# Kernel tuning notes

Hardware: AMD Instinct MI355X
Metric: run time of the kernel (lower is better)

Reference implementation:

```python
import jax, jax.numpy as jnp
import numpy as np
from jax import lax

# Production-scale RPN detection-head config
B, FH, FW, NA = 8, 200, 200, 9      # batch, fmap h, fmap w, anchors/cell
H, W = 800, 800                      # image dims
N = FH * FW * NA                     # 360k anchors per image
NMS_THR = 0.7
MIN_SIZE = 1e-3


def _make_anchors():
    scales = np.array([32.0, 64.0, 128.0])
    ratios = np.array([0.5, 1.0, 2.0])
    ws = (scales[:, None] * np.sqrt(1.0 / ratios)[None, :]).reshape(-1)  # [NA]
    hs = (scales[:, None] * np.sqrt(ratios)[None, :]).reshape(-1)
    sy, sx = H / FH, W / FW
    cx = (np.arange(FW) + 0.5) * sx
    cy = (np.arange(FH) + 0.5) * sy
    cxg, cyg = np.meshgrid(cx, cy)                     # [FH,FW]
    cxg = cxg[..., None]; cyg = cyg[..., None]         # [FH,FW,1]
    a = np.stack([cxg - ws / 2, cyg - hs / 2, cxg + ws / 2, cyg + hs / 2], axis=-1)
    return jnp.asarray(a.reshape(-1, 4), jnp.float32)  # [N,4] xyxy


def setup_inputs() -> dict:
    key = jax.random.key(0)
    k1, k2 = jax.random.split(key)
    cls_logits = jax.random.normal(k1, (B, N, 1), jnp.float32)
    reg_deltas = jax.random.normal(k2, (B, N, 4), jnp.float32) * 0.1  # sane exp(dw)
    anchors = jnp.broadcast_to(_make_anchors()[None], (B, N, 4))
    return {
        "cls_logits": cls_logits,
        "reg_deltas": reg_deltas,
        "anchors": anchors,
        "keep_pre_nms": 1000,
        "keep_post_nms": 300,
    }


def _offsets2boxes(deltas, anchors):
    aw = anchors[:, 2] - anchors[:, 0]
    ah = anchors[:, 3] - anchors[:, 1]
    acx = anchors[:, 0] + 0.5 * aw
    acy = anchors[:, 1] + 0.5 * ah
    cx = deltas[:, 0] * aw + acx
    cy = deltas[:, 1] * ah + acy
    w = jnp.exp(deltas[:, 2]) * aw
    h = jnp.exp(deltas[:, 3]) * ah
    return jnp.stack([cx - 0.5 * w, cy - 0.5 * h, cx + 0.5 * w, cy + 0.5 * h], axis=-1)


def _iou_matrix(b):
    area = (b[:, 2] - b[:, 0]) * (b[:, 3] - b[:, 1])
    lt = jnp.maximum(b[:, None, :2], b[None, :, :2])
    rb = jnp.minimum(b[:, None, 2:], b[None, :, 2:])
    wh = jnp.clip(rb - lt, 0.0)
    inter = wh[..., 0] * wh[..., 1]
    return inter / (area[:, None] + area[None, :] - inter + 1e-9)


def _detect_one(logit, delta, anc, pre, post):
    scores = jax.nn.sigmoid(logit.reshape(-1))             # [N]
    boxes = _offsets2boxes(delta.reshape(-1, 4), anc)      # [N,4]
    s, idx = lax.top_k(scores, pre)                        # sorted desc
    b = boxes[idx]                                         # [pre,4]
    # clip to image
    b = jnp.stack([
        jnp.clip(b[:, 0], 0.0, W), jnp.clip(b[:, 1], 0.0, H),
        jnp.clip(b[:, 2], 0.0, W), jnp.clip(b[:, 3], 0.0, H)], axis=-1)
    valid = ((b[:, 2] - b[:, 0]) >= MIN_SIZE) & ((b[:, 3] - b[:, 1]) >= MIN_SIZE)
    # greedy NMS on score-sorted boxes (mask-based, fixed shapes)
    iou = _iou_matrix(lax.stop_gradient(b))                # [pre,pre]
    j = jnp.arange(pre)

    def body(keep, i):
        sup = (iou[i] > NMS_THR) & (j > i) & keep[i]
        return keep & ~sup, None

    keep, _ = lax.scan(body, valid, jnp.arange(pre))
    # compact first `post` kept detections into fixed [post,5], zero-padded
    dets = jnp.concatenate([b, s[:, None]], axis=-1)       # [pre,5]
    rank = jnp.cumsum(keep) - 1
    tgt = jnp.where(keep & (rank < post), rank, post)
    out = jnp.zeros((post + 1, 5), dets.dtype).at[tgt].set(dets)[:post]
    return out


def reference(cls_logits, reg_deltas, anchors, keep_pre_nms, keep_post_nms):
    f = lambda l, d, a: _detect_one(l, d, a, keep_pre_nms, keep_post_nms)
    return jax.vmap(f)(cls_logits, reg_deltas, anchors)    # [B,post,5]
```

## Files before the change

kernel.cpp:

```cpp
#include <hip/hip_runtime.h>
#include <stdint.h>
#include <math.h>

typedef unsigned long long u64;
typedef unsigned int u32;

#define NPI   360000
#define B_IMG 8
#define PRE   1000
#define POST  300
#define CAP   4096
#define NMSF  0.7f
#define IMG_W 800.0f
#define IMG_H 800.0f

#define NBIN    8192
#define KSHIFT  19
#define CHUNK_H 36
#define F4PB_H  (NPI / 4 / CHUNK_H)
#define CHUNK_C 48
#define F4PB_C  (NPI / 4 / CHUNK_C)
#define EPB_C   (NPI / CHUNK_C)
#define LBUF    1024

#define CNT_OFF    0
#define THRESH_OFF 128
#define VALID_OFF  256
#define RHIST_OFF  4096
#define ZERO_BYTES 266240
#define BOX_OFF    266240
#define SCORE_OFF  394240
#define CAND_OFF   426240
#define MASK_OFF   688384

__device__ __forceinline__ u32 fkey(float f) {
  u32 u = __float_as_uint(f);
  return (u & 0x80000000u) ? ~u : (u | 0x80000000u);
}
__device__ __forceinline__ u64 rl64(u64 v, int lane) {
  u32 lo = (u32)__builtin_amdgcn_readlane((int)(u32)v, lane);
  u32 hi = (u32)__builtin_amdgcn_readlane((int)(u32)(v >> 32), lane);
  return ((u64)hi << 32) | lo;
}
__device__ __forceinline__ u64 sx64(u64 v, int m) {
  u32 lo = (u32)__shfl_xor((int)(u32)v, m, 64);
  u32 hi = (u32)__shfl_xor((int)(u32)(v >> 32), m, 64);
  return ((u64)hi << 32) | lo;
}

__global__ __launch_bounds__(256) void k_hist(const float* __restrict__ logits,
                                              u32* __restrict__ rhist) {
  __shared__ u32 h[NBIN];
  const int img = blockIdx.y, c = blockIdx.x;
  for (int i = threadIdx.x; i < NBIN; i += 256) h[i] = 0;
  __syncthreads();
  const float4* L = (const float4*)(logits + (size_t)img * NPI) + (size_t)c * F4PB_H;
  for (int i = threadIdx.x; i < F4PB_H; i += 256) {
    float4 v = L[i];
    atomicAdd(&h[fkey(v.x) >> KSHIFT], 1u);
    atomicAdd(&h[fkey(v.y) >> KSHIFT], 1u);
    atomicAdd(&h[fkey(v.z) >> KSHIFT], 1u);
    atomicAdd(&h[fkey(v.w) >> KSHIFT], 1u);
  }
  __syncthreads();
  u32* R = rhist + img * NBIN;
  for (int i = threadIdx.x; i < NBIN; i += 256) {
    u32 cn = h[i];
    if (cn) atomicAdd(&R[i], cn);
  }
}

__global__ __launch_bounds__(1024) void k_select(const u32* __restrict__ rhist,
                                                 int* __restrict__ thresh) {
  const int img = blockIdx.x;
  const int t = threadIdx.x;
  const int lane = t & 63, w = t >> 6;
  const uint4* H4 = (const uint4*)(rhist + img * NBIN);
  uint4 v0 = H4[2 * t], v1 = H4[2 * t + 1];
  u32 binc[8] = {v0.x, v0.y, v0.z, v0.w, v1.x, v1.y, v1.z, v1.w};
  u32 s = 0;
#pragma unroll
  for (int b = 0; b < 8; b++) s += binc[b];
  u32 suf = s;
#pragma unroll
  for (int off = 1; off < 64; off <<= 1) {
    u32 o = (u32)__shfl_down((int)suf, off, 64);
    if (lane + off < 64) suf += o;
  }
  __shared__ u32 wtot[16];
  if (lane == 0) wtot[w] = suf;
  __syncthreads();
  u32 wsuf = 0;
  for (int ww = w + 1; ww < 16; ww++) wsuf += wtot[ww];
  u32 suffix_incl = suf + wsuf;
  u32 s_excl = suffix_incl - s;
  if (suffix_incl >= (u32)PRE && s_excl < (u32)PRE) {
    u32 cum = s_excl;
    int bin = 8 * t;
#pragma unroll
    for (int b = 7; b >= 0; b--) {
      cum += binc[b];
      if (cum >= (u32)PRE) { bin = 8 * t + b; break; }
    }
    thresh[img] = bin;
  }
}

__global__ __launch_bounds__(256) void k_compact(const float* __restrict__ logits,
                                                 const int* __restrict__ thresh,
                                                 u32* __restrict__ cnt,
                                                 u64* __restrict__ cand) {
  __shared__ u64 buf[LBUF];
  __shared__ u32 bcnt;
  __shared__ u32 gbase;
  const int img = blockIdx.y, c = blockIdx.x;
  const int tb  = thresh[img];
  if (threadIdx.x == 0) bcnt = 0;
  __syncthreads();
  const float4* L = (const float4*)(logits + (size_t)img * NPI) + (size_t)c * F4PB_C;
  const int ebase = c * EPB_C;
  for (int i = threadIdx.x; i < F4PB_C; i += 256) {
    float4 v = L[i];
    float xs[4] = {v.x, v.y, v.z, v.w};
#pragma unroll
    for (int q = 0; q < 4; q++) {
      float x = xs[q];
      if ((int)(fkey(x) >> KSHIFT) >= tb) {
        float ef = (float)exp(-(double)x);
        float sg = 1.0f / (1.0f + ef);
        u32 e = (u32)(ebase + 4 * i + q);
        u32 p = atomicAdd(&bcnt, 1u);
        if (p < LBUF)
          buf[p] = ((u64)fkey(sg) << 32) | (u64)(0xFFFFFFFFu - e);
      }
    }
  }
  __syncthreads();
  if (threadIdx.x == 0) {
    u32 m = bcnt < LBUF ? bcnt : LBUF;
    bcnt = m;
    gbase = atomicAdd(&cnt[img], m);
  }
  __syncthreads();
  const u32 m = bcnt, gb = gbase;
  for (u32 j = threadIdx.x; j < m; j += 256) {
    u32 pos = gb + j;
    if (pos < CAP) cand[img * CAP + pos] = buf[j];
  }
}

#define RB 8
__device__ __forceinline__ void emit_row(
    int img, int row, u64 key,
    const float* __restrict__ deltas, const float* __restrict__ anchors,
    float4* __restrict__ boxes, float* __restrict__ scores, u64* __restrict__ validw) {
  u32 hi  = (u32)(key >> 32);
  u32 idx = 0xFFFFFFFFu - (u32)(key & 0xFFFFFFFFu);
  u32 su  = (hi & 0x80000000u) ? (hi ^ 0x80000000u) : ~hi;
  float sc = __uint_as_float(su);
  size_t off = (size_t)img * NPI + idx;
  float4 d = ((const float4*)deltas)[off];
  float4 a = ((const float4*)anchors)[off];
  float aw = a.z - a.x, ah = a.w - a.y;
  float acx = a.x + 0.5f * aw, acy = a.y + 0.5f * ah;
  float cx = d.x * aw + acx, cy = d.y * ah + acy;
  float w = expf(d.z) * aw, h = expf(d.w) * ah;
  float x1 = cx - 0.5f * w, y1 = cy - 0.5f * h;
  float x2 = cx + 0.5f * w, y2 = cy + 0.5f * h;
  x1 = fminf(fmaxf(x1, 0.f), IMG_W);
  y1 = fminf(fmaxf(y1, 0.f), IMG_H);
  x2 = fminf(fmaxf(x2, 0.f), IMG_W);
  y2 = fminf(fmaxf(y2, 0.f), IMG_H);
  boxes[img * PRE + row]  = make_float4(x1, y1, x2, y2);
  scores[img * PRE + row] = sc;
  if (((x2 - x1) >= 1e-3f) && ((y2 - y1) >= 1e-3f))
    atomicOr(&validw[img * 16 + (row >> 6)], 1ull << (row & 63));
}

__global__ __launch_bounds__(256) void k_rank(
    const float* __restrict__ deltas, const float* __restrict__ anchors,
    const u32* __restrict__ cnt, const u64* __restrict__ cand,
    float4* __restrict__ boxes, float* __restrict__ scores, u64* __restrict__ validw) {
  __shared__ u64 skey[CAP];
  const int img = blockIdx.y;
  int n = (int)cnt[img];
  if (n > CAP) n = CAP;
  for (int i = threadIdx.x; i < n; i += 256) skey[i] = cand[img * CAP + i];
  __syncthreads();
  const int r0 = blockIdx.x * 256 + threadIdx.x;
  const int r1 = r0 + RB * 256;
  u64 k0 = (r0 < n) ? skey[r0] : 0ull;
  u64 k1 = (r1 < n) ? skey[r1] : 0ull;
  int c0 = 0, c1 = 0;
  for (int j = 0; j < n; j++) {
    u64 kj = skey[j];
    c0 += (kj > k0);
    c1 += (kj > k1);
  }
  if (r0 < n && c0 < PRE) emit_row(img, c0, k0, deltas, anchors, boxes, scores, validw);
  if (r1 < n && c1 < PRE) emit_row(img, c1, k1, deltas, anchors, boxes, scores, validw);
}

__global__ __launch_bounds__(1024) void k_iou(const float4* __restrict__ boxes,
                                              u64* __restrict__ mask) {
  __shared__ float4 sb[1024];
  __shared__ float  sa[1024];
  const int img = blockIdx.y;
  const int tid = threadIdx.x;
  {
    float4 b = (tid < PRE) ? boxes[img * PRE + tid]
                           : make_float4(0.f, 0.f, 0.f, 0.f);
    sb[tid] = b;
    sa[tid] = (b.z - b.x) * (b.w - b.y);
  }
  __syncthreads();
  const int lane = tid & 63;
  const int wv   = tid >> 6;
  const int i    = blockIdx.x * 64 + lane;
  const bool rowok = (i < PRE);
  const float4 bi = sb[blockIdx.x * 64 + lane];
  const float  ai = sa[blockIdx.x * 64 + lane];
  const int cbase = wv << 6;
  u64 bits = 0;
#pragma unroll
  for (int k = 0; k < 64; k++) {
    int c = cbase + k;
    float4 bc = sb[c];
    float ac  = sa[c];
    float ltx = fmaxf(bi.x, bc.x), lty = fmaxf(bi.y, bc.y);
    float rbx = fminf(bi.z, bc.z), rby = fminf(bi.w, bc.w);
    float iw = fmaxf(rbx - ltx, 0.f), ih = fmaxf(rby - lty, 0.f);
    float inter = iw * ih;
    float iou = inter / (ai + ac - inter + 1e-9f);
    bits |= (iou > NMSF) ? (1ull << k) : 0ull;
  }
  int d = i - cbase;
  u64 gtmask = (d < 0) ? ~0ull : ((d >= 63) ? 0ull : (~0ull << (d + 1)));
  int rem = PRE - cbase;
  u64 tmask = (rem >= 64) ? ~0ull : ((rem <= 0) ? 0ull : ((1ull << rem) - 1ull));
  bits &= gtmask & tmask;
  if (rowok) mask[((size_t)img * PRE + i) * 16 + wv] = bits;
}

#define LDSROWS 496
#define NMS_T   320
__global__ __launch_bounds__(NMS_T) void k_nms(
    const u64* __restrict__ mask, const u64* __restrict__ validw,
    const float4* __restrict__ boxes, const float* __restrict__ scores,
    float* __restrict__ out) {
  __shared__ u64 smask[LDSROWS * 16];
  __shared__ int skeeplist[POST];
  __shared__ int skept;
  const int img = blockIdx.x;
  const int tid = threadIdx.x;
  const u64* M = mask + (size_t)img * PRE * 16;
  u64 diag[16];
  if (tid < 64) {
#pragma unroll
    for (int cc = 0; cc < 16; cc++) {
      int row = cc * 64 + tid;
      diag[cc] = (row < PRE) ? M[(size_t)row * 16 + cc] : 0ull;
    }
  }
  for (int e = tid; e < LDSROWS * 16; e += NMS_T) smask[e] = M[e];
  __syncthreads();
  if (tid < 64) {
    const int lane = tid;
    const int w = lane & 15, g = lane >> 4;
    u64 rem = ~0ull;
    if (lane < 16) {
      rem = ~validw[img * 16 + lane];
      if (lane == 15) rem |= 0xFFFFFF0000000000ull;
    }
    int kept = 0;
#pragma unroll
    for (int cc = 0; cc < 16; cc++) {
      u64 alive = ~rl64(rem, cc);
      int kept0 = kept;
      while (alive != 0ull && kept < POST) {
        int r = __builtin_ctzll(alive);
        if (lane == 0) skeeplist[kept] = cc * 64 + r;
        kept++;
        u64 sup = rl64(diag[cc], r);
        alive &= ~sup;
        alive &= ~(1ull << r);
      }
      int nc = kept - kept0;
      if (nc > 0 && kept < POST && cc < 15) {
        u64 part = 0;
        for (int j = g; j < nc; j += 4) {
          int row = skeeplist[kept0 + j];
          part |= (row < LDSROWS) ? smask[row * 16 + w] : M[(size_t)row * 16 + w];
        }
        part |= sx64(part, 16);
        part |= sx64(part, 32);
        rem |= part;
      }
      if (kept >= POST) break;
    }
    if (lane == 0) skept = kept;
  }
  __syncthreads();
  if (tid < POST) {
    float4 bx = make_float4(0.f, 0.f, 0.f, 0.f);
    float  sc = 0.f;
    if (tid < skept) {
      int i = skeeplist[tid];
      bx = boxes[img * PRE + i];
      sc = scores[img * PRE + i];
    }
    float* o = out + ((size_t)img * POST + tid) * 5;
    o[0] = bx.x; o[1] = bx.y; o[2] = bx.z; o[3] = bx.w; o[4] = sc;
  }
}

extern "C" void kernel_launch(void* const* d_in, const int* in_sizes, int n_in,
                              void* d_out, int out_size, void* d_ws, size_t ws_size,
                              hipStream_t stream) {
  const float* logits  = (const float*)d_in[0];
  const float* deltas  = (const float*)d_in[1];
  const float* anchors = (const float*)d_in[2];
  float* out = (float*)d_out;
  char* ws = (char*)d_ws;

  u32* cnt      = (u32*)(ws + CNT_OFF);
  int* thresh   = (int*)(ws + THRESH_OFF);
  u64* validw   = (u64*)(ws + VALID_OFF);
  u32* rhist    = (u32*)(ws + RHIST_OFF);
  float4* boxes = (float4*)(ws + BOX_OFF);
  float* scores = (float*)(ws + SCORE_OFF);
  u64* cand     = (u64*)(ws + CAND_OFF);
  u64* mask     = (u64*)(ws + MASK_OFF);

  hipMemsetAsync(ws, 0, ZERO_BYTES, stream);
  dim3 gh(CHUNK_H, B_IMG);
  k_hist<<<gh, 256, 0, stream>>>(logits, rhist);
  k_select<<<B_IMG, 1024, 0, stream>>>(rhist, thresh);
  dim3 gc(CHUNK_C, B_IMG);
  k_compact<<<gc, 256, 0, stream>>>(logits, thresh, cnt, cand);
  dim3 gr(RB, B_IMG);
  k_rank<<<gr, 256, 0, stream>>>(deltas, anchors, cnt, cand, boxes, scores, validw);
  dim3 g2(16, B_IMG);
  k_iou<<<g2, 1024, 0, stream>>>(boxes, mask);
  k_nms<<<B_IMG, NMS_T, 0, stream>>>(mask, validw, boxes, scores, out);
}
```

Before: 210.9 us.

## Fuse pipeline into single cooperative persistent kernel with grid syncs

Replaces the memset plus six kernel launches with one cooperative kernel of 256 blocks that runs histogram, threshold select, compaction, rank/decode, IoU mask and NMS as phases separated by grid.sync, sharing one LDS union. The aim is to remove launch gaps and the memset. The phases are also re-partitioned: 32 rank blocks instead of 64 and 256 IoU blocks instead of 128, and select runs with 256 threads. Costs include grid-wide barriers, only 256 blocks for the memory-bound histogram/compaction passes, and a large LDS union that limits occupancy. The original multi-kernel path is kept as a fallback if the cooperative launch fails.

Result: slower. 485.7 us (+130.3%).

```diff
diff --git a/kernel.cpp b/kernel.cpp
--- a/kernel.cpp
+++ b/kernel.cpp
@@ -1,6 +1,9 @@
 #include <hip/hip_runtime.h>
+#include <hip/hip_cooperative_groups.h>
 #include <stdint.h>
 #include <math.h>
+
+namespace cg = cooperative_groups;
 
 typedef unsigned long long u64;
 typedef unsigned int u32;
@@ -33,6 +36,10 @@
 #define CAND_OFF   426240
 #define MASK_OFF   688384
 
+#define LDSROWS 496
+#define NMS_T   320
+#define FGRID   256
+
 __device__ __forceinline__ u32 fkey(float f) {
   u32 u = __float_as_uint(f);
   return (u & 0x80000000u) ? ~u : (u | 0x80000000u);
@@ -48,108 +55,6 @@
   return ((u64)hi << 32) | lo;
 }
 
-__global__ __launch_bounds__(256) void k_hist(const float* __restrict__ logits,
-                                              u32* __restrict__ rhist) {
-  __shared__ u32 h[NBIN];
-  const int img = blockIdx.y, c = blockIdx.x;
-  for (int i = threadIdx.x; i < NBIN; i += 256) h[i] = 0;
-  __syncthreads();
-  const float4* L = (const float4*)(logits + (size_t)img * NPI) + (size_t)c * F4PB_H;
-  for (int i = threadIdx.x; i < F4PB_H; i += 256) {
-    float4 v = L[i];
-    atomicAdd(&h[fkey(v.x) >> KSHIFT], 1u);
-    atomicAdd(&h[fkey(v.y) >> KSHIFT], 1u);
-    atomicAdd(&h[fkey(v.z) >> KSHIFT], 1u);
-    atomicAdd(&h[fkey(v.w) >> KSHIFT], 1u);
-  }
-  __syncthreads();
-  u32* R = rhist + img * NBIN;
-  for (int i = threadIdx.x; i < NBIN; i += 256) {
-    u32 cn = h[i];
-    if (cn) atomicAdd(&R[i], cn);
-  }
-}
-
-__global__ __launch_bounds__(1024) void k_select(const u32* __restrict__ rhist,
-                                                 int* __restrict__ thresh) {
-  const int img = blockIdx.x;
-  const int t = threadIdx.x;
-  const int lane = t & 63, w = t >> 6;
-  const uint4* H4 = (const uint4*)(rhist + img * NBIN);
-  uint4 v0 = H4[2 * t], v1 = H4[2 * t + 1];
-  u32 binc[8] = {v0.x, v0.y, v0.z, v0.w, v1.x, v1.y, v1.z, v1.w};
-  u32 s = 0;
-#pragma unroll
-  for (int b = 0; b < 8; b++) s += binc[b];
-  u32 suf = s;
-#pragma unroll
-  for (int off = 1; off < 64; off <<= 1) {
-    u32 o = (u32)__shfl_down((int)suf, off, 64);
-    if (lane + off < 64) suf += o;
-  }
-  __shared__ u32 wtot[16];
-  if (lane == 0) wtot[w] = suf;
-  __syncthreads();
-  u32 wsuf = 0;
-  for (int ww = w + 1; ww < 16; ww++) wsuf += wtot[ww];
-  u32 suffix_incl = suf + wsuf;
-  u32 s_excl = suffix_incl - s;
-  if (suffix_incl >= (u32)PRE && s_excl < (u32)PRE) {
-    u32 cum = s_excl;
-    int bin = 8 * t;
-#pragma unroll
-    for (int b = 7; b >= 0; b--) {
-      cum += binc[b];
-      if (cum >= (u32)PRE) { bin = 8 * t + b; break; }
-    }
-    thresh[img] = bin;
-  }
-}
-
-__global__ __launch_bounds__(256) void k_compact(const float* __restrict__ logits,
-                                                 const int* __restrict__ thresh,
-                                                 u32* __restrict__ cnt,
-                                                 u64* __restrict__ cand) {
-  __shared__ u64 buf[LBUF];
-  __shared__ u32 bcnt;
-  __shared__ u32 gbase;
-  const int img = blockIdx.y, c = blockIdx.x;
-  const int tb  = thresh[img];
-  if (threadIdx.x == 0) bcnt = 0;
-  __syncthreads();
-  const float4* L = (const float4*)(logits + (size_t)img * NPI) + (size_t)c * F4PB_C;
-  const int ebase = c * EPB_C;
-  for (int i = threadIdx.x; i < F4PB_C; i += 256) {
-    float4 v = L[i];
-    float xs[4] = {v.x, v.y, v.z, v.w};
-#pragma unroll
-    for (int q = 0; q < 4; q++) {
-      float x = xs[q];
-      if ((int)(fkey(x) >> KSHIFT) >= tb) {
-        float ef = (float)exp(-(double)x);
-        float sg = 1.0f / (1.0f + ef);
-        u32 e = (u32)(ebase + 4 * i + q);
-        u32 p = atomicAdd(&bcnt, 1u);
-        if (p < LBUF)
-          buf[p] = ((u64)fkey(sg) << 32) | (u64)(0xFFFFFFFFu - e);
-      }
-    }
-  }
-  __syncthreads();
-  if (threadIdx.x == 0) {
-    u32 m = bcnt < LBUF ? bcnt : LBUF;
-    bcnt = m;
-    gbase = atomicAdd(&cnt[img], m);
-  }
-  __syncthreads();
-  const u32 m = bcnt, gb = gbase;
-  for (u32 j = threadIdx.x; j < m; j += 256) {
-    u32 pos = gb + j;
-    if (pos < CAP) cand[img * CAP + pos] = buf[j];
-  }
-}
-
-#define RB 8
 __device__ __forceinline__ void emit_row(
     int img, int row, u64 key,
     const float* __restrict__ deltas, const float* __restrict__ anchors,
@@ -177,6 +82,370 @@
     atomicOr(&validw[img * 16 + (row >> 6)], 1ull << (row & 63));
 }
 
+__global__ __launch_bounds__(256) void k_fused(
+    const float* __restrict__ logits, const float* __restrict__ deltas,
+    const float* __restrict__ anchors,
+    u32* __restrict__ cnt, int* __restrict__ thresh, u64* __restrict__ validw,
+    u32* __restrict__ rhist, float4* __restrict__ boxes, float* __restrict__ scores,
+    u64* __restrict__ cand, u64* __restrict__ mask, float* __restrict__ out) {
+  __shared__ union {
+    u32 hist[NBIN];
+    u32 wtot[4];
+    struct { u64 buf[LBUF]; u32 bcnt; u32 gbase; } comp;
+    u64 skey[CAP];
+    struct { float4 sb[1024]; float sa[1024]; } iou;
+    struct { u64 smask[LDSROWS * 16]; int keeplist[POST]; int kept; } nms;
+  } lds;
+  cg::grid_group grid = cg::this_grid();
+  const int bid = blockIdx.x, tid = threadIdx.x;
+
+  {
+    int g = bid * 256 + tid;
+    rhist[g] = 0;
+    if (g < B_IMG) cnt[g] = 0;
+    if (g < B_IMG * 16) validw[g] = 0;
+  }
+  __threadfence();
+  grid.sync();
+
+  for (int u = bid; u < B_IMG * CHUNK_H; u += FGRID) {
+    const int img = u / CHUNK_H, c = u % CHUNK_H;
+    for (int i = tid; i < NBIN; i += 256) lds.hist[i] = 0;
+    __syncthreads();
+    const float4* L = (const float4*)(logits + (size_t)img * NPI) + (size_t)c * F4PB_H;
+    for (int i = tid; i < F4PB_H; i += 256) {
+      float4 v = L[i];
+      atomicAdd(&lds.hist[fkey(v.x) >> KSHIFT], 1u);
+      atomicAdd(&lds.hist[fkey(v.y) >> KSHIFT], 1u);
+      atomicAdd(&lds.hist[fkey(v.z) >> KSHIFT], 1u);
+      atomicAdd(&lds.hist[fkey(v.w) >> KSHIFT], 1u);
+    }
+    __syncthreads();
+    u32* R = rhist + img * NBIN;
+    for (int i = tid; i < NBIN; i += 256) {
+      u32 cv = lds.hist[i];
+      if (cv) atomicAdd(&R[i], cv);
+    }
+    __syncthreads();
+  }
+  __threadfence();
+  grid.sync();
+
+  if (bid < B_IMG) {
+    const int img = bid, t = tid;
+    const int lane = t & 63, w = t >> 6;
+    const uint4* H4 = (const uint4*)(rhist + img * NBIN);
+    u32 binc[32];
+    u32 s = 0;
+#pragma unroll
+    for (int q = 0; q < 8; q++) {
+      uint4 v = H4[8 * t + q];
+      binc[4 * q + 0] = v.x; binc[4 * q + 1] = v.y;
+      binc[4 * q + 2] = v.z; binc[4 * q + 3] = v.w;
+      s += v.x + v.y + v.z + v.w;
+    }
+    u32 suf = s;
+#pragma unroll
+    for (int off = 1; off < 64; off <<= 1) {
+      u32 o = (u32)__shfl_down((int)suf, off, 64);
+      if (lane + off < 64) suf += o;
+    }
+    if (lane == 0) lds.wtot[w] = suf;
+    __syncthreads();
+    u32 wsuf = 0;
+    for (int ww = w + 1; ww < 4; ww++) wsuf += lds.wtot[ww];
+    u32 suffix_incl = suf + wsuf;
+    u32 s_excl = suffix_incl - s;
+    if (suffix_incl >= (u32)PRE && s_excl < (u32)PRE) {
+      u32 cum = s_excl;
+      int bin = 32 * t;
+#pragma unroll
+      for (int b = 31; b >= 0; b--) {
+        cum += binc[b];
+        if (cum >= (u32)PRE) { bin = 32 * t + b; break; }
+      }
+      thresh[img] = bin;
+    }
+  }
+  __threadfence();
+  grid.sync();
+
+  for (int u = bid; u < B_IMG * CHUNK_C; u += FGRID) {
+    const int img = u / CHUNK_C, c = u % CHUNK_C;
+    const int tb = thresh[img];
+    if (tid == 0) lds.comp.bcnt = 0;
+    __syncthreads();
+    const float4* L = (const float4*)(logits + (size_t)img * NPI) + (size_t)c * F4PB_C;
+    const int ebase = c * EPB_C;
+    for (int i = tid; i < F4PB_C; i += 256) {
+      float4 v = L[i];
+      float xs[4] = {v.x, v.y, v.z, v.w};
+#pragma unroll
+      for (int q = 0; q < 4; q++) {
+        float x = xs[q];
+        if ((int)(fkey(x) >> KSHIFT) >= tb) {
+          float ef = (float)exp(-(double)x);
+          float sg = 1.0f / (1.0f + ef);
+          u32 e = (u32)(ebase + 4 * i + q);
+          u32 p = atomicAdd(&lds.comp.bcnt, 1u);
+          if (p < LBUF)
+            lds.comp.buf[p] = ((u64)fkey(sg) << 32) | (u64)(0xFFFFFFFFu - e);
+        }
+      }
+    }
+    __syncthreads();
+    if (tid == 0) {
+      u32 m = lds.comp.bcnt < LBUF ? lds.comp.bcnt : LBUF;
+      lds.comp.bcnt = m;
+      lds.comp.gbase = atomicAdd(&cnt[img], m);
+    }
+    __syncthreads();
+    const u32 m = lds.comp.bcnt, gb = lds.comp.gbase;
+    for (u32 j = tid; j < m; j += 256) {
+      u32 pos = gb + j;
+      if (pos < CAP) cand[img * CAP + pos] = lds.comp.buf[j];
+    }
+    __syncthreads();
+  }
+  __threadfence();
+  grid.sync();
+
+  if (bid < 4 * B_IMG) {
+    const int img = bid >> 2, part = bid & 3;
+    int n = (int)cnt[img];
+    if (n > CAP) n = CAP;
+    for (int i = tid; i < n; i += 256) lds.skey[i] = cand[img * CAP + i];
+    __syncthreads();
+    if (part * 1024 < n) {
+      const int r0 = part * 1024 + tid;
+      const int r1 = r0 + 256, r2 = r0 + 512, r3 = r0 + 768;
+      u64 k0 = (r0 < n) ? lds.skey[r0] : 0ull;
+      u64 k1 = (r1 < n) ? lds.skey[r1] : 0ull;
+      u64 k2 = (r2 < n) ? lds.skey[r2] : 0ull;
+      u64 k3 = (r3 < n) ? lds.skey[r3] : 0ull;
+      int c0 = 0, c1 = 0, c2 = 0, c3 = 0;
+      for (int j = 0; j < n; j++) {
+        u64 kj = lds.skey[j];
+        c0 += (kj > k0); c1 += (kj > k1); c2 += (kj > k2); c3 += (kj > k3);
+      }
+      if (r0 < n && c0 < PRE) emit_row(img, c0, k0, deltas, anchors, boxes, scores, validw);
+      if (r1 < n && c1 < PRE) emit_row(img, c1, k1, deltas, anchors, boxes, scores, validw);
+      if (r2 < n && c2 < PRE) emit_row(img, c2, k2, deltas, anchors, boxes, scores, validw);
+      if (r3 < n && c3 < PRE) emit_row(img, c3, k3, deltas, anchors, boxes, scores, validw);
+    }
+  }
+  __threadfence();
+  grid.sync();
+
+  {
+    const int img = bid >> 5, rb = bid & 31;
+    for (int j = tid; j < 1024; j += 256) {
+      float4 b = (j < PRE) ? boxes[img * PRE + j] : make_float4(0.f, 0.f, 0.f, 0.f);
+      lds.iou.sb[j] = b;
+      lds.iou.sa[j] = (b.z - b.x) * (b.w - b.y);
+    }
+    __syncthreads();
+    const int i = rb * 32 + (tid & 31);
+    const int wq = tid >> 5;
+    const bool rowok = (i < PRE);
+    const float4 bi = lds.iou.sb[i];
+    const float  ai = lds.iou.sa[i];
+#pragma unroll
+    for (int hh = 0; hh < 2; hh++) {
+      const int wv = wq + 8 * hh;
+      const int cbase = wv << 6;
+      u64 bits = 0;
+#pragma unroll
+      for (int k = 0; k < 64; k++) {
+        int c = cbase + k;
+        float4 bc = lds.iou.sb[c];
+        float ac  = lds.iou.sa[c];
+        float ltx = fmaxf(bi.x, bc.x), lty = fmaxf(bi.y, bc.y);
+        float rbx = fminf(bi.z, bc.z), rby = fminf(bi.w, bc.w);
+        float iw = fmaxf(rbx - ltx, 0.f), ih = fmaxf(rby - lty, 0.f);
+        float inter = iw * ih;
+        float iou = inter / (ai + ac - inter + 1e-9f);
+        bits |= (iou > NMSF) ? (1ull << k) : 0ull;
+      }
+      int d = i - cbase;
+      u64 gtmask = (d < 0) ? ~0ull : ((d >= 63) ? 0ull : (~0ull << (d + 1)));
+      int rem = PRE - cbase;
+      u64 tmask = (rem >= 64) ? ~0ull : ((rem <= 0) ? 0ull : ((1ull << rem) - 1ull));
+      bits &= gtmask & tmask;
+      if (rowok) mask[((size_t)img * PRE + i) * 16 + wv] = bits;
+    }
+  }
+  __threadfence();
+  grid.sync();
+
+  if (bid < B_IMG) {
+    const int img = bid;
+    const u64* M = mask + (size_t)img * PRE * 16;
+    u64 diag[16];
+    if (tid < 64) {
+#pragma unroll
+      for (int cc = 0; cc < 16; cc++) {
+        int row = cc * 64 + tid;
+        diag[cc] = (row < PRE) ? M[(size_t)row * 16 + cc] : 0ull;
+      }
+    }
+    for (int e = tid; e < LDSROWS * 16; e += 256) lds.nms.smask[e] = M[e];
+    __syncthreads();
+    if (tid < 64) {
+      const int lane = tid;
+      const int w = lane & 15, g = lane >> 4;
+      u64 rem = ~0ull;
+      if (lane < 16) {
+        rem = ~validw[img * 16 + lane];
+        if (lane == 15) rem |= 0xFFFFFF0000000000ull;
+      }
+      int kept = 0;
+#pragma unroll
+      for (int cc = 0; cc < 16; cc++) {
+        u64 alive = ~rl64(rem, cc);
+        int kept0 = kept;
+        while (alive != 0ull && kept < POST) {
+          int r = __builtin_ctzll(alive);
+          if (lane == 0) lds.nms.keeplist[kept] = cc * 64 + r;
+          kept++;
+          u64 sup = rl64(diag[cc], r);
+          alive &= ~sup;
+          alive &= ~(1ull << r);
+        }
+        int nc = kept - kept0;
+        if (nc > 0 && kept < POST && cc < 15) {
+          u64 part = 0;
+          for (int j = g; j < nc; j += 4) {
+            int row = lds.nms.keeplist[kept0 + j];
+            part |= (row < LDSROWS) ? lds.nms.smask[row * 16 + w]
+                                    : M[(size_t)row * 16 + w];
+          }
+          part |= sx64(part, 16);
+          part |= sx64(part, 32);
+          rem |= part;
+        }
+        if (kept >= POST) break;
+      }
+      if (lane == 0) lds.nms.kept = kept;
+    }
+    __syncthreads();
+    for (int o = tid; o < POST; o += 256) {
+      float4 bx = make_float4(0.f, 0.f, 0.f, 0.f);
+      float  sc = 0.f;
+      if (o < lds.nms.kept) {
+        int i2 = lds.nms.keeplist[o];
+        bx = boxes[img * PRE + i2];
+        sc = scores[img * PRE + i2];
+      }
+      float* op = out + ((size_t)img * POST + o) * 5;
+      op[0] = bx.x; op[1] = bx.y; op[2] = bx.z; op[3] = bx.w; op[4] = sc;
+    }
+  }
+}
+
+
+__global__ __launch_bounds__(256) void k_hist(const float* __restrict__ logits,
+                                              u32* __restrict__ rhist) {
+  __shared__ u32 h[NBIN];
+  const int img = blockIdx.y, c = blockIdx.x;
+  for (int i = threadIdx.x; i < NBIN; i += 256) h[i] = 0;
+  __syncthreads();
+  const float4* L = (const float4*)(logits + (size_t)img * NPI) + (size_t)c * F4PB_H;
+  for (int i = threadIdx.x; i < F4PB_H; i += 256) {
+    float4 v = L[i];
+    atomicAdd(&h[fkey(v.x) >> KSHIFT], 1u);
+    atomicAdd(&h[fkey(v.y) >> KSHIFT], 1u);
+    atomicAdd(&h[fkey(v.z) >> KSHIFT], 1u);
+    atomicAdd(&h[fkey(v.w) >> KSHIFT], 1u);
+  }
+  __syncthreads();
+  u32* R = rhist + img * NBIN;
+  for (int i = threadIdx.x; i < NBIN; i += 256) {
+    u32 cn = h[i];
+    if (cn) atomicAdd(&R[i], cn);
+  }
+}
+
+__global__ __launch_bounds__(1024) void k_select(const u32* __restrict__ rhist,
+                                                 int* __restrict__ thresh) {
+  const int img = blockIdx.x;
+  const int t = threadIdx.x;
+  const int lane = t & 63, w = t >> 6;
+  const uint4* H4 = (const uint4*)(rhist + img * NBIN);
+  uint4 v0 = H4[2 * t], v1 = H4[2 * t + 1];
+  u32 binc[8] = {v0.x, v0.y, v0.z, v0.w, v1.x, v1.y, v1.z, v1.w};
+  u32 s = 0;
+#pragma unroll
+  for (int b = 0; b < 8; b++) s += binc[b];
+  u32 suf = s;
+#pragma unroll
+  for (int off = 1; off < 64; off <<= 1) {
+    u32 o = (u32)__shfl_down((int)suf, off, 64);
+    if (lane + off < 64) suf += o;
+  }
+  __shared__ u32 wtot[16];
+  if (lane == 0) wtot[w] = suf;
+  __syncthreads();
+  u32 wsuf = 0;
+  for (int ww = w + 1; ww < 16; ww++) wsuf += wtot[ww];
+  u32 suffix_incl = suf + wsuf;
+  u32 s_excl = suffix_incl - s;
+  if (suffix_incl >= (u32)PRE && s_excl < (u32)PRE) {
+    u32 cum = s_excl;
+    int bin = 8 * t;
+#pragma unroll
+    for (int b = 7; b >= 0; b--) {
+      cum += binc[b];
+      if (cum >= (u32)PRE) { bin = 8 * t + b; break; }
+    }
+    thresh[img] = bin;
+  }
+}
+
+__global__ __launch_bounds__(256) void k_compact(const float* __restrict__ logits,
+                                                 const int* __restrict__ thresh,
+                                                 u32* __restrict__ cnt,
+                                                 u64* __restrict__ cand) {
+  __shared__ u64 buf[LBUF];
+  __shared__ u32 bcnt;
+  __shared__ u32 gbase;
+  const int img = blockIdx.y, c = blockIdx.x;
+  const int tb  = thresh[img];
+  if (threadIdx.x == 0) bcnt = 0;
+  __syncthreads();
+  const float4* L = (const float4*)(logits + (size_t)img * NPI) + (size_t)c * F4PB_C;
+  const int ebase = c * EPB_C;
+  for (int i = threadIdx.x; i < F4PB_C; i += 256) {
+    float4 v = L[i];
+    float xs[4] = {v.x, v.y, v.z, v.w};
+#pragma unroll
+    for (int q = 0; q < 4; q++) {
+      float x = xs[q];
+      if ((int)(fkey(x) >> KSHIFT) >= tb) {
+        float ef = (float)exp(-(double)x);
+        float sg = 1.0f / (1.0f + ef);
+        u32 e = (u32)(ebase + 4 * i + q);
+        u32 p = atomicAdd(&bcnt, 1u);
+        if (p < LBUF)
+          buf[p] = ((u64)fkey(sg) << 32) | (u64)(0xFFFFFFFFu - e);
+      }
+    }
+  }
+  __syncthreads();
+  if (threadIdx.x == 0) {
+    u32 m = bcnt < LBUF ? bcnt : LBUF;
+    bcnt = m;
+    gbase = atomicAdd(&cnt[img], m);
+  }
+  __syncthreads();
+  const u32 m = bcnt, gb = gbase;
+  for (u32 j = threadIdx.x; j < m; j += 256) {
+    u32 pos = gb + j;
+    if (pos < CAP) cand[img * CAP + pos] = buf[j];
+  }
+}
+
+#define RB 8
 __global__ __launch_bounds__(256) void k_rank(
     const float* __restrict__ deltas, const float* __restrict__ anchors,
     const u32* __restrict__ cnt, const u64* __restrict__ cand,
@@ -242,8 +511,6 @@
   if (rowok) mask[((size_t)img * PRE + i) * 16 + wv] = bits;
 }
 
-#define LDSROWS 496
-#define NMS_T   320
 __global__ __launch_bounds__(NMS_T) void k_nms(
     const u64* __restrict__ mask, const u64* __restrict__ validw,
     const float4* __restrict__ boxes, const float* __restrict__ scores,
@@ -332,15 +599,23 @@
   u64* cand     = (u64*)(ws + CAND_OFF);
   u64* mask     = (u64*)(ws + MASK_OFF);
 
-  hipMemsetAsync(ws, 0, ZERO_BYTES, stream);
-  dim3 gh(CHUNK_H, B_IMG);
-  k_hist<<<gh, 256, 0, stream>>>(logits, rhist);
-  k_select<<<B_IMG, 1024, 0, stream>>>(rhist, thresh);
-  dim3 gc(CHUNK_C, B_IMG);
-  k_compact<<<gc, 256, 0, stream>>>(logits, thresh, cnt, cand);
-  dim3 gr(RB, B_IMG);
-  k_rank<<<gr, 256, 0, stream>>>(deltas, anchors, cnt, cand, boxes, scores, validw);
-  dim3 g2(16, B_IMG);
-  k_iou<<<g2, 1024, 0, stream>>>(boxes, mask);
-  k_nms<<<B_IMG, NMS_T, 0, stream>>>(mask, validw, boxes, scores, out);
-}
+  void* args[] = {(void*)&logits, (void*)&deltas, (void*)&anchors,
+                  (void*)&cnt, (void*)&thresh, (void*)&validw, (void*)&rhist,
+                  (void*)&boxes, (void*)&scores, (void*)&cand, (void*)&mask,
+                  (void*)&out};
+  hipError_t err = hipLaunchCooperativeKernel((void*)k_fused, dim3(FGRID), dim3(256),
+                                              args, 0, stream);
+  if (err != hipSuccess) {
+    hipMemsetAsync(ws, 0, ZERO_BYTES, stream);
+    dim3 gh(CHUNK_H, B_IMG);
+    k_hist<<<gh, 256, 0, stream>>>(logits, rhist);
+    k_select<<<B_IMG, 1024, 0, stream>>>(rhist, thresh);
+    dim3 gc(CHUNK_C, B_IMG);
+    k_compact<<<gc, 256, 0, stream>>>(logits, thresh, cnt, cand);
+    dim3 gr(RB, B_IMG);
+    k_rank<<<gr, 256, 0, stream>>>(deltas, anchors, cnt, cand, boxes, scores, validw);
+    dim3 g2(16, B_IMG);
+    k_iou<<<g2, 1024, 0, stream>>>(boxes, mask);
+    k_nms<<<B_IMG, NMS_T, 0, stream>>>(mask, validw, boxes, scores, out);
+  }
+}
```

## Fuse threshold selection into compaction and drop memset via per-block histograms

Applied to the files above, without the earlier changes.

The histogram kernel now writes per-block partial histograms plus coarse group sums instead of atomically merging into a global histogram. Each compaction block then recomputes the top-PRE threshold bin with a two-level coarse/fine scan. This removes the separate select kernel and the workspace memset, since the histogram kernel zeroes the counters itself. The cost is redundant threshold computation in every compaction block, extra reads of the partial histograms, and a coarser bin count that may let more candidates through.

Result: no change. 207.1 us (-1.8%).

```diff
diff --git a/kernel.cpp b/kernel.cpp
--- a/kernel.cpp
+++ b/kernel.cpp
@@ -14,24 +14,27 @@
 #define IMG_W 800.0f
 #define IMG_H 800.0f
 
-#define NBIN    8192
-#define KSHIFT  19
-#define CHUNK_H 36
+#define NBIN    4096
+#define KSHIFT  20
+#define NGRP    64
+#define CHUNK_H 30
 #define F4PB_H  (NPI / 4 / CHUNK_H)
 #define CHUNK_C 48
 #define F4PB_C  (NPI / 4 / CHUNK_C)
 #define EPB_C   (NPI / CHUNK_C)
 #define LBUF    1024
 
-#define CNT_OFF    0
-#define THRESH_OFF 128
-#define VALID_OFF  256
-#define RHIST_OFF  4096
-#define ZERO_BYTES 266240
-#define BOX_OFF    266240
-#define SCORE_OFF  394240
-#define CAND_OFF   426240
-#define MASK_OFF   688384
+#define CNT_OFF     0
+#define VALID_OFF   256
+#define PHIST_OFF   4096
+#define PCOARSE_OFF 3936256
+#define BOX_OFF     3997696
+#define SCORE_OFF   4125696
+#define CAND_OFF    4157696
+#define MASK_OFF    4419840
+
+#define LDSROWS 496
+#define NMS_T   320
 
 __device__ __forceinline__ u32 fkey(float f) {
   u32 u = __float_as_uint(f);
@@ -49,13 +52,17 @@
 }
 
 __global__ __launch_bounds__(256) void k_hist(const float* __restrict__ logits,
-                                              u32* __restrict__ rhist) {
+                                              u32* __restrict__ phist,
+                                              u32* __restrict__ pcoarse,
+                                              u32* __restrict__ cnt,
+                                              u64* __restrict__ validw) {
   __shared__ u32 h[NBIN];
   const int img = blockIdx.y, c = blockIdx.x;
-  for (int i = threadIdx.x; i < NBIN; i += 256) h[i] = 0;
+  const int tid = threadIdx.x;
+  for (int i = tid; i < NBIN; i += 256) h[i] = 0;
   __syncthreads();
   const float4* L = (const float4*)(logits + (size_t)img * NPI) + (size_t)c * F4PB_H;
-  for (int i = threadIdx.x; i < F4PB_H; i += 256) {
+  for (int i = tid; i < F4PB_H; i += 256) {
     float4 v = L[i];
     atomicAdd(&h[fkey(v.x) >> KSHIFT], 1u);
     atomicAdd(&h[fkey(v.y) >> KSHIFT], 1u);
@@ -63,63 +70,66 @@
     atomicAdd(&h[fkey(v.w) >> KSHIFT], 1u);
   }
   __syncthreads();
-  u32* R = rhist + img * NBIN;
-  for (int i = threadIdx.x; i < NBIN; i += 256) {
-    u32 cn = h[i];
-    if (cn) atomicAdd(&R[i], cn);
-  }
-}
-
-__global__ __launch_bounds__(1024) void k_select(const u32* __restrict__ rhist,
-                                                 int* __restrict__ thresh) {
-  const int img = blockIdx.x;
-  const int t = threadIdx.x;
-  const int lane = t & 63, w = t >> 6;
-  const uint4* H4 = (const uint4*)(rhist + img * NBIN);
-  uint4 v0 = H4[2 * t], v1 = H4[2 * t + 1];
-  u32 binc[8] = {v0.x, v0.y, v0.z, v0.w, v1.x, v1.y, v1.z, v1.w};
-  u32 s = 0;
-#pragma unroll
-  for (int b = 0; b < 8; b++) s += binc[b];
-  u32 suf = s;
-#pragma unroll
-  for (int off = 1; off < 64; off <<= 1) {
-    u32 o = (u32)__shfl_down((int)suf, off, 64);
-    if (lane + off < 64) suf += o;
-  }
-  __shared__ u32 wtot[16];
-  if (lane == 0) wtot[w] = suf;
-  __syncthreads();
-  u32 wsuf = 0;
-  for (int ww = w + 1; ww < 16; ww++) wsuf += wtot[ww];
-  u32 suffix_incl = suf + wsuf;
-  u32 s_excl = suffix_incl - s;
-  if (suffix_incl >= (u32)PRE && s_excl < (u32)PRE) {
-    u32 cum = s_excl;
-    int bin = 8 * t;
-#pragma unroll
-    for (int b = 7; b >= 0; b--) {
-      cum += binc[b];
-      if (cum >= (u32)PRE) { bin = 8 * t + b; break; }
-    }
-    thresh[img] = bin;
+  u32* P = phist + ((size_t)img * CHUNK_H + c) * NBIN;
+  for (int i = tid; i < NBIN; i += 256) P[i] = h[i];
+  if (tid < NGRP) {
+    u32 s = 0;
+#pragma unroll
+    for (int b = 0; b < NBIN / NGRP; b++) s += h[tid * (NBIN / NGRP) + b];
+    pcoarse[((size_t)img * CHUNK_H + c) * NGRP + tid] = s;
+  }
+  if (c == 0) {
+    if (tid < 16) validw[img * 16 + tid] = 0;
+    if (img == 0 && tid < B_IMG) cnt[tid] = 0;
   }
 }
 
 __global__ __launch_bounds__(256) void k_compact(const float* __restrict__ logits,
-                                                 const int* __restrict__ thresh,
+                                                 const u32* __restrict__ phist,
+                                                 const u32* __restrict__ pcoarse,
                                                  u32* __restrict__ cnt,
                                                  u64* __restrict__ cand) {
   __shared__ u64 buf[LBUF];
   __shared__ u32 bcnt;
   __shared__ u32 gbase;
+  __shared__ int stb;
   const int img = blockIdx.y, c = blockIdx.x;
-  const int tb  = thresh[img];
-  if (threadIdx.x == 0) bcnt = 0;
-  __syncthreads();
+  const int t = threadIdx.x;
+  if (t == 0) { bcnt = 0; stb = 0; }
+  if (t < 64) {
+    const u32* PC = pcoarse + (size_t)img * CHUNK_H * NGRP;
+    u32 cg = 0;
+    for (int cc = 0; cc < CHUNK_H; cc++) cg += PC[cc * NGRP + t];
+    u32 suf = cg;
+#pragma unroll
+    for (int off = 1; off < 64; off <<= 1) {
+      u32 o = (u32)__shfl_down((int)suf, off, 64);
+      if (t + off < 64) suf += o;
+    }
+    u32 sx = suf - cg;
+    u64 bal = __ballot(suf >= (u32)PRE && sx < (u32)PRE);
+    if (bal) {
+      int gc = __builtin_ctzll(bal);
+      u32 s_above = (u32)__shfl((int)sx, gc, 64);
+      const u32* P = phist + (size_t)img * CHUNK_H * NBIN + gc * (NBIN / NGRP);
+      u32 fb = 0;
+      for (int cc = 0; cc < CHUNK_H; cc++) fb += P[(size_t)cc * NBIN + t];
+      u32 fsuf = fb;
+#pragma unroll
+      for (int off = 1; off < 64; off <<= 1) {
+        u32 o = (u32)__shfl_down((int)fsuf, off, 64);
+        if (t + off < 64) fsuf += o;
+      }
+      u32 fincl = fsuf + s_above;
+      u32 fexcl = fincl - fb;
+      if (fincl >= (u32)PRE && fexcl < (u32)PRE) stb = gc * (NBIN / NGRP) + t;
+    }
+  }
+  __syncthreads();
+  const int tb = stb;
   const float4* L = (const float4*)(logits + (size_t)img * NPI) + (size_t)c * F4PB_C;
   const int ebase = c * EPB_C;
-  for (int i = threadIdx.x; i < F4PB_C; i += 256) {
+  for (int i = t; i < F4PB_C; i += 256) {
     float4 v = L[i];
     float xs[4] = {v.x, v.y, v.z, v.w};
 #pragma unroll
@@ -136,20 +146,19 @@
     }
   }
   __syncthreads();
-  if (threadIdx.x == 0) {
+  if (t == 0) {
     u32 m = bcnt < LBUF ? bcnt : LBUF;
     bcnt = m;
     gbase = atomicAdd(&cnt[img], m);
   }
   __syncthreads();
   const u32 m = bcnt, gb = gbase;
-  for (u32 j = threadIdx.x; j < m; j += 256) {
+  for (u32 j = t; j < m; j += 256) {
     u32 pos = gb + j;
     if (pos < CAP) cand[img * CAP + pos] = buf[j];
   }
 }
 
-#define RB 8
 __device__ __forceinline__ void emit_row(
     int img, int row, u64 key,
     const float* __restrict__ deltas, const float* __restrict__ anchors,
@@ -177,6 +186,7 @@
     atomicOr(&validw[img * 16 + (row >> 6)], 1ull << (row & 63));
 }
 
+#define RB 8
 __global__ __launch_bounds__(256) void k_rank(
     const float* __restrict__ deltas, const float* __restrict__ anchors,
     const u32* __restrict__ cnt, const u64* __restrict__ cand,
@@ -242,8 +252,6 @@
   if (rowok) mask[((size_t)img * PRE + i) * 16 + wv] = bits;
 }
 
-#define LDSROWS 496
-#define NMS_T   320
 __global__ __launch_bounds__(NMS_T) void k_nms(
     const u64* __restrict__ mask, const u64* __restrict__ validw,
     const float4* __restrict__ boxes, const float* __restrict__ scores,
@@ -324,20 +332,18 @@
   char* ws = (char*)d_ws;
 
   u32* cnt      = (u32*)(ws + CNT_OFF);
-  int* thresh   = (int*)(ws + THRESH_OFF);
   u64* validw   = (u64*)(ws + VALID_OFF);
-  u32* rhist    = (u32*)(ws + RHIST_OFF);
+  u32* phist    = (u32*)(ws + PHIST_OFF);
+  u32* pcoarse  = (u32*)(ws + PCOARSE_OFF);
   float4* boxes = (float4*)(ws + BOX_OFF);
   float* scores = (float*)(ws + SCORE_OFF);
   u64* cand     = (u64*)(ws + CAND_OFF);
   u64* mask     = (u64*)(ws + MASK_OFF);
 
-  hipMemsetAsync(ws, 0, ZERO_BYTES, stream);
   dim3 gh(CHUNK_H, B_IMG);
-  k_hist<<<gh, 256, 0, stream>>>(logits, rhist);
-  k_select<<<B_IMG, 1024, 0, stream>>>(rhist, thresh);
+  k_hist<<<gh, 256, 0, stream>>>(logits, phist, pcoarse, cnt, validw);
   dim3 gc(CHUNK_C, B_IMG);
-  k_compact<<<gc, 256, 0, stream>>>(logits, thresh, cnt, cand);
+  k_compact<<<gc, 256, 0, stream>>>(logits, phist, pcoarse, cnt, cand);
   dim3 gr(RB, B_IMG);
   k_rank<<<gr, 256, 0, stream>>>(deltas, anchors, cnt, cand, boxes, scores, validw);
   dim3 g2(16, B_IMG);
```
